# Performance work log

Hardware: AMD Instinct MI355X
Metric: run time of the kernel (lower is better)

Reference implementation:

```python
import jax, jax.numpy as jnp
import numpy as np

B, S, DM, H, HD, I, MAXREL = 4, 1024, 1024, 16, 64, 4096, 10
LN_EPS = 1e-3  # keras LayerNormalization default


def gelu(x):
    # tanh approximation from arXiv:1606.08415, as in the source
    return x * 0.5 * (1.0 + jnp.tanh(np.sqrt(2.0 / np.pi) * (x + 0.044715 * x ** 3)))


def layernorm(x, g, b):
    m = jnp.mean(x, axis=-1, keepdims=True)
    v = jnp.mean((x - m) ** 2, axis=-1, keepdims=True)
    return (x - m) * jax.lax.rsqrt(v + LN_EPS) * g + b


def setup_inputs() -> dict:
    key = jax.random.key(0)
    ks = jax.random.split(key, 12)
    sc = 0.02
    inp = {
        'x': jax.random.normal(ks[0], (B, S, DM), dtype=jnp.float32),
        'mask': jax.random.randint(ks[1], (B, S), 0, 2, dtype=jnp.int32),
        'Wqk': jax.random.normal(ks[2], (DM, H * HD), dtype=jnp.float32) * sc,
        'bqk': jnp.zeros((H * HD,), dtype=jnp.float32),
        'Wv': jax.random.normal(ks[3], (DM, H * HD), dtype=jnp.float32) * sc,
        'bv': jnp.zeros((H * HD,), dtype=jnp.float32),
        'rel_emb': jax.random.normal(ks[4], (2 * MAXREL + 1, HD), dtype=jnp.float32) * sc,
        'Wap': jax.random.normal(ks[5], (H * HD, DM), dtype=jnp.float32) * sc,
        'bap': jnp.zeros((DM,), dtype=jnp.float32),
        'g1': jnp.ones((DM,), dtype=jnp.float32),
        'b1': jnp.zeros((DM,), dtype=jnp.float32),
        'Wi': jax.random.normal(ks[6], (DM, I), dtype=jnp.float32) * sc,
        'bi': jnp.zeros((I,), dtype=jnp.float32),
        'Wo': jax.random.normal(ks[7], (I, DM), dtype=jnp.float32) * sc,
        'bo': jnp.zeros((DM,), dtype=jnp.float32),
        'g2': jnp.ones((DM,), dtype=jnp.float32),
        'b2': jnp.zeros((DM,), dtype=jnp.float32),
    }
    return inp


def _forward(x, mask, Wqk, bqk, Wv, bv, rel_emb, Wap, bap, g1, b1, Wi, bi, Wo, bo, g2, b2):
    b, s, _ = x.shape
    # shared query/key projection (qk_layer used for both q and k)
    qk = (x @ Wqk + bqk).reshape(b, s, H, HD).transpose(0, 2, 1, 3)  # [B,H,S,D]
    v = (x @ Wv + bv).reshape(b, s, H, HD).transpose(0, 2, 1, 3)
    # relative position ids: distance[i,j] = j - i, clipped to +-MAXREL, shifted
    r = jnp.arange(s)
    rel_idx = jnp.clip(r[None, :] - r[:, None], -MAXREL, MAXREL) + MAXREL  # [S,S]
    rel_k = rel_emb[rel_idx]  # [S,S,D]
    # Eq. 4 of arXiv:1803.02155 (note: no 1/sqrt(d) scaling in relative path)
    scores = jnp.einsum('bhqd,bhkd->bhqk', qk, qk) + jnp.einsum('bhqd,qkd->bhqk', qk, rel_k)
    # attention mask with self-exclusion (subtract identity, clip to [0,1])
    m = mask.astype(jnp.float32)  # [B,S]
    amask = jnp.clip(jnp.ones((b, s, 1), jnp.float32) * m[:, None, :] - jnp.eye(s), 0.0, 1.0)
    scores = scores + (1.0 - amask[:, None]) * -10000.0
    probs = jax.nn.softmax(scores, axis=-1)  # [B,H,S,S]
    ctx = jnp.einsum('bhqk,bhkd->bhqd', probs, v).transpose(0, 2, 1, 3).reshape(b, s, H * HD)
    # attention projection: Dense+gelu, residual, LN
    attn_out = layernorm(gelu(ctx @ Wap + bap) + x, g1, b1)
    inter = gelu(attn_out @ Wi + bi)
    out = layernorm(gelu(inter @ Wo + bo) + attn_out, g2, b2)
    return out, probs


def reference(x, mask, Wqk, bqk, Wv, bv, rel_emb, Wap, bap, g1, b1, Wi, bi, Wo, bo, g2, b2):
    return _forward(x, mask, Wqk, bqk, Wv, bv, rel_emb, Wap, bap, g1, b1, Wi, bi, Wo, bo, g2, b2)
```

## Files before the change

kernel.cpp:

```cpp
#include <hip/hip_runtime.h>
#include <hip/hip_bf16.h>

#define B_  4
#define S_  1024
#define DM_ 1024
#define H_  16
#define HD_ 64
#define I_  4096

typedef __attribute__((ext_vector_type(8))) short bf16x8;
typedef __attribute__((ext_vector_type(4))) float f32x4;

__device__ __forceinline__ float gelu_f(float x) {
  float x3 = x * x * x;
  return 0.5f * x * (1.0f + tanhf(0.7978845608028654f * (x + 0.044715f * x3)));
}

__device__ __forceinline__ unsigned short f32_to_bf16(float f) {
  unsigned int u = __float_as_uint(f);
  unsigned int rounding = 0x7FFFu + ((u >> 16) & 1u);
  u += rounding;
  return (unsigned short)(u >> 16);
}

__device__ __forceinline__ float bf16_to_f32(unsigned short u) {
  return __uint_as_float(((unsigned int)u) << 16);
}

__device__ __forceinline__ void split_bf16(float v, unsigned short& h, unsigned short& l) {
  h = f32_to_bf16(v);
  l = f32_to_bf16(v - bf16_to_f32(h));
}

__global__ __launch_bounds__(256) void cvt_bf16_kernel(
    const float* __restrict__ in, unsigned short* __restrict__ out, int n4)
{
  int i = blockIdx.x * 256 + threadIdx.x;
  if (i < n4) {
    float4 v = *reinterpret_cast<const float4*>(&in[(size_t)i * 4]);
    ushort4 o;
    o.x = f32_to_bf16(v.x); o.y = f32_to_bf16(v.y);
    o.z = f32_to_bf16(v.z); o.w = f32_to_bf16(v.w);
    *reinterpret_cast<ushort4*>(&out[(size_t)i * 4]) = o;
  }
}

__global__ __launch_bounds__(256) void tcvt_kernel(
    const float* __restrict__ W, unsigned short* __restrict__ WT, int K, int N)
{
  __shared__ float tile[64][65];
  const int tid = threadIdx.x;
  const int k0 = blockIdx.y * 64, n0 = blockIdx.x * 64;
#pragma unroll
  for (int i = 0; i < 4; ++i) {
    int u = tid + i * 256;
    int kr = u >> 4, nc = (u & 15) * 4;
    float4 v = *reinterpret_cast<const float4*>(&W[(size_t)(k0 + kr) * N + n0 + nc]);
    tile[kr][nc + 0] = v.x; tile[kr][nc + 1] = v.y;
    tile[kr][nc + 2] = v.z; tile[kr][nc + 3] = v.w;
  }
  __syncthreads();
  int n = tid >> 2, ks = (tid & 3) * 16;
  unsigned short* dst = &WT[(size_t)(n0 + n) * K + k0 + ks];
#pragma unroll
  for (int j = 0; j < 4; ++j) {
    ushort4 o;
    o.x = f32_to_bf16(tile[ks + j * 4 + 0][n]);
    o.y = f32_to_bf16(tile[ks + j * 4 + 1][n]);
    o.z = f32_to_bf16(tile[ks + j * 4 + 2][n]);
    o.w = f32_to_bf16(tile[ks + j * 4 + 3][n]);
    *reinterpret_cast<ushort4*>(&dst[j * 4]) = o;
  }
}

__global__ __launch_bounds__(256) void t_f32_kernel(
    const float* __restrict__ W, float* __restrict__ WT, int K, int N)
{
  __shared__ float tile[64][65];
  const int tid = threadIdx.x;
  const int k0 = blockIdx.y * 64, n0 = blockIdx.x * 64;
#pragma unroll
  for (int i = 0; i < 4; ++i) {
    int u = tid + i * 256;
    int kr = u >> 4, nc = (u & 15) * 4;
    float4 v = *reinterpret_cast<const float4*>(&W[(size_t)(k0 + kr) * N + n0 + nc]);
    tile[kr][nc + 0] = v.x; tile[kr][nc + 1] = v.y;
    tile[kr][nc + 2] = v.z; tile[kr][nc + 3] = v.w;
  }
  __syncthreads();
  int n = tid >> 2, ks = (tid & 3) * 16;
  float* dst = &WT[(size_t)(n0 + n) * K + k0 + ks];
#pragma unroll
  for (int j = 0; j < 4; ++j) {
    float4 o = make_float4(tile[ks + j * 4 + 0][n], tile[ks + j * 4 + 1][n],
                           tile[ks + j * 4 + 2][n], tile[ks + j * 4 + 3][n]);
    *reinterpret_cast<float4*>(&dst[j * 4]) = o;
  }
}

template<bool GELU, bool RES, bool RESBF16, bool BHSD, bool OBF16>
__global__ __launch_bounds__(256) void gemm_mfma_kernel(
    const unsigned short* __restrict__ A, const unsigned short* __restrict__ BT,
    const float* __restrict__ bias, const void* __restrict__ res,
    void* __restrict__ C, int M, int N, int K)
{
  __shared__ unsigned short As[128][40];
  __shared__ unsigned short Bs[128][40];
  const int tid = threadIdx.x;
  const int wid = tid >> 6;
  const int lane = tid & 63;
  const int bm = blockIdx.y * 128;
  const int bn = blockIdx.x * 128;
  const int l15 = lane & 15;
  const int kb = (lane >> 4) * 8;

  f32x4 acc[2][8];
#pragma unroll
  for (int mi = 0; mi < 2; ++mi)
#pragma unroll
    for (int ni = 0; ni < 8; ++ni) acc[mi][ni] = (f32x4){0.f, 0.f, 0.f, 0.f};

  for (int k0 = 0; k0 < K; k0 += 32) {
#pragma unroll
    for (int i = 0; i < 2; ++i) {
      int u = tid + i * 256;
      int row = u >> 2, seg = (u & 3) * 8;
      int4 va = *reinterpret_cast<const int4*>(&A[(size_t)(bm + row) * K + k0 + seg]);
      *reinterpret_cast<int4*>(&As[row][seg]) = va;
      int4 vb = *reinterpret_cast<const int4*>(&BT[(size_t)(bn + row) * K + k0 + seg]);
      *reinterpret_cast<int4*>(&Bs[row][seg]) = vb;
    }
    __syncthreads();

    bf16x8 af[2], bf[8];
#pragma unroll
    for (int mi = 0; mi < 2; ++mi)
      af[mi] = *reinterpret_cast<const bf16x8*>(&As[wid * 32 + mi * 16 + l15][kb]);
#pragma unroll
    for (int ni = 0; ni < 8; ++ni)
      bf[ni] = *reinterpret_cast<const bf16x8*>(&Bs[ni * 16 + l15][kb]);
#pragma unroll
    for (int mi = 0; mi < 2; ++mi)
#pragma unroll
      for (int ni = 0; ni < 8; ++ni)
        acc[mi][ni] = __builtin_amdgcn_mfma_f32_16x16x32_bf16(
            af[mi], bf[ni], acc[mi][ni], 0, 0, 0);
    __syncthreads();
  }

#pragma unroll
  for (int mi = 0; mi < 2; ++mi) {
#pragma unroll
    for (int ni = 0; ni < 8; ++ni) {
      int gcol = bn + ni * 16 + l15;
      float bsv = bias[gcol];
#pragma unroll
      for (int r = 0; r < 4; ++r) {
        int grow = bm + wid * 32 + mi * 16 + (lane >> 4) * 4 + r;
        float val = acc[mi][ni][r] + bsv;
        if (GELU) val = gelu_f(val);
        if (RES) {
          if (RESBF16) val += bf16_to_f32(((const unsigned short*)res)[(size_t)grow * N + gcol]);
          else         val += ((const float*)res)[(size_t)grow * N + gcol];
        }
        if (BHSD) {
          int bb = grow >> 10, ss = grow & 1023, hh = gcol >> 6, dd = gcol & 63;
          size_t adr = ((size_t)(bb * H_ + hh) * S_ + ss) * HD_ + dd;
          if (OBF16) ((unsigned short*)C)[adr] = f32_to_bf16(val);
          else       ((float*)C)[adr] = val;
        } else if (OBF16) {
          ((unsigned short*)C)[(size_t)grow * N + gcol] = f32_to_bf16(val);
        } else {
          ((float*)C)[(size_t)grow * N + gcol] = val;
        }
      }
    }
  }
}

__global__ __launch_bounds__(256) void gemm_mfma3_kernel(
    const float* __restrict__ A, const float* __restrict__ BT,
    const float* __restrict__ bias, float* __restrict__ C, int M, int N, int K)
{
  __shared__ unsigned short Ah[128][40], Al[128][40];
  __shared__ unsigned short Bh[128][40], Bl[128][40];
  const int tid = threadIdx.x;
  const int wid = tid >> 6;
  const int lane = tid & 63;
  const int bm = blockIdx.y * 128;
  const int bn = blockIdx.x * 128;
  const int l15 = lane & 15;
  const int kb = (lane >> 4) * 8;

  f32x4 acc[2][8];
#pragma unroll
  for (int mi = 0; mi < 2; ++mi)
#pragma unroll
    for (int ni = 0; ni < 8; ++ni) acc[mi][ni] = (f32x4){0.f, 0.f, 0.f, 0.f};

  for (int k0 = 0; k0 < K; k0 += 32) {
#pragma unroll
    for (int i = 0; i < 2; ++i) {
      int u = tid + i * 256;
      int row = u >> 2, seg = (u & 3) * 8;
#pragma unroll
      for (int half = 0; half < 2; ++half) {
        float4 va = *reinterpret_cast<const float4*>(&A[(size_t)(bm + row) * K + k0 + seg + half * 4]);
        ushort4 h4, l4;
        split_bf16(va.x, h4.x, l4.x); split_bf16(va.y, h4.y, l4.y);
        split_bf16(va.z, h4.z, l4.z); split_bf16(va.w, h4.w, l4.w);
        *reinterpret_cast<ushort4*>(&Ah[row][seg + half * 4]) = h4;
        *reinterpret_cast<ushort4*>(&Al[row][seg + half * 4]) = l4;
        float4 vb = *reinterpret_cast<const float4*>(&BT[(size_t)(bn + row) * K + k0 + seg + half * 4]);
        split_bf16(vb.x, h4.x, l4.x); split_bf16(vb.y, h4.y, l4.y);
        split_bf16(vb.z, h4.z, l4.z); split_bf16(vb.w, h4.w, l4.w);
        *reinterpret_cast<ushort4*>(&Bh[row][seg + half * 4]) = h4;
        *reinterpret_cast<ushort4*>(&Bl[row][seg + half * 4]) = l4;
      }
    }
    __syncthreads();

    bf16x8 ah[2], al[2];
#pragma unroll
    for (int mi = 0; mi < 2; ++mi) {
      ah[mi] = *reinterpret_cast<const bf16x8*>(&Ah[wid * 32 + mi * 16 + l15][kb]);
      al[mi] = *reinterpret_cast<const bf16x8*>(&Al[wid * 32 + mi * 16 + l15][kb]);
    }
#pragma unroll
    for (int ni = 0; ni < 8; ++ni) {
      bf16x8 bh = *reinterpret_cast<const bf16x8*>(&Bh[ni * 16 + l15][kb]);
      bf16x8 bl = *reinterpret_cast<const bf16x8*>(&Bl[ni * 16 + l15][kb]);
#pragma unroll
      for (int mi = 0; mi < 2; ++mi) {
        acc[mi][ni] = __builtin_amdgcn_mfma_f32_16x16x32_bf16(ah[mi], bh, acc[mi][ni], 0, 0, 0);
        acc[mi][ni] = __builtin_amdgcn_mfma_f32_16x16x32_bf16(al[mi], bh, acc[mi][ni], 0, 0, 0);
        acc[mi][ni] = __builtin_amdgcn_mfma_f32_16x16x32_bf16(ah[mi], bl, acc[mi][ni], 0, 0, 0);
      }
    }
    __syncthreads();
  }

#pragma unroll
  for (int mi = 0; mi < 2; ++mi) {
#pragma unroll
    for (int ni = 0; ni < 8; ++ni) {
      int gcol = bn + ni * 16 + l15;
      float bsv = bias[gcol];
#pragma unroll
      for (int r = 0; r < 4; ++r) {
        int grow = bm + wid * 32 + mi * 16 + (lane >> 4) * 4 + r;
        float val = acc[mi][ni][r] + bsv;
        int bb = grow >> 10, ss = grow & 1023, hh = gcol >> 6, dd = gcol & 63;
        C[((size_t)(bb * H_ + hh) * S_ + ss) * HD_ + dd] = val;
      }
    }
  }
}

__global__ __launch_bounds__(256) void attn_mfma_kernel(
    const float* __restrict__ qk, const int* __restrict__ mask,
    const float* __restrict__ rel_emb, float* __restrict__ probs)
{
  __shared__ unsigned short Qh[16][72], Ql[16][72];
  __shared__ float Qf[16][68];
  __shared__ unsigned short Kh[128][72], Kl[128][72];
  __shared__ float relp[16][21];
  __shared__ float red1[4][16], red2[4][16];
  __shared__ int msk[1024];

  const int tid = threadIdx.x;
  const int b = blockIdx.z, h = blockIdx.y, qt = blockIdx.x;
  const float* qkbh = qk + (size_t)(b * H_ + h) * S_ * HD_;
  const int q0 = qt * 16;

  for (int i = tid; i < 1024; i += 256) msk[i] = mask[b * S_ + i];

  {
    int row = tid >> 4, dq = (tid & 15) * 4;
    float4 v = *reinterpret_cast<const float4*>(&qkbh[(size_t)(q0 + row) * HD_ + dq]);
    Qf[row][dq + 0] = v.x; Qf[row][dq + 1] = v.y;
    Qf[row][dq + 2] = v.z; Qf[row][dq + 3] = v.w;
    ushort4 h4, l4;
    split_bf16(v.x, h4.x, l4.x); split_bf16(v.y, h4.y, l4.y);
    split_bf16(v.z, h4.z, l4.z); split_bf16(v.w, h4.w, l4.w);
    *reinterpret_cast<ushort4*>(&Qh[row][dq]) = h4;
    *reinterpret_cast<ushort4*>(&Ql[row][dq]) = l4;
  }
  __syncthreads();

  for (int idx = tid; idx < 16 * 21; idx += 256) {
    int q = idx / 21, r = idx - q * 21;
    float s = 0.f;
#pragma unroll 8
    for (int d = 0; d < 64; ++d) s += Qf[q][d] * rel_emb[r * 64 + d];
    relp[q][r] = s;
  }

  const int wv = tid >> 6;
  const int lane = tid & 63;
  const int l15 = lane & 15;
  const int hi4 = lane >> 4;
  const int kb = hi4 * 8;

  bf16x8 ah[2], al[2];
#pragma unroll
  for (int ks = 0; ks < 2; ++ks) {
    ah[ks] = *reinterpret_cast<const bf16x8*>(&Qh[l15][ks * 32 + kb]);
    al[ks] = *reinterpret_cast<const bf16x8*>(&Ql[l15][ks * 32 + kb]);
  }

  f32x4 acc[8][2];
#pragma unroll
  for (int t = 0; t < 8; ++t)
#pragma unroll
    for (int f = 0; f < 2; ++f) acc[t][f] = (f32x4){0.f, 0.f, 0.f, 0.f};

#pragma unroll
  for (int kt = 0; kt < 8; ++kt) {
    __syncthreads();
#pragma unroll
    for (int i = 0; i < 8; ++i) {
      int u = tid + i * 256;
      int row = u >> 4, dq = (u & 15) * 4;
      float4 v = *reinterpret_cast<const float4*>(&qkbh[(size_t)(kt * 128 + row) * HD_ + dq]);
      ushort4 h4, l4;
      split_bf16(v.x, h4.x, l4.x); split_bf16(v.y, h4.y, l4.y);
      split_bf16(v.z, h4.z, l4.z); split_bf16(v.w, h4.w, l4.w);
      *reinterpret_cast<ushort4*>(&Kh[row][dq]) = h4;
      *reinterpret_cast<ushort4*>(&Kl[row][dq]) = l4;
    }
    __syncthreads();

#pragma unroll
    for (int f = 0; f < 2; ++f) {
      int cb = wv * 32 + f * 16;
#pragma unroll
      for (int ks = 0; ks < 2; ++ks) {
        bf16x8 bh = *reinterpret_cast<const bf16x8*>(&Kh[cb + l15][ks * 32 + kb]);
        bf16x8 bl = *reinterpret_cast<const bf16x8*>(&Kl[cb + l15][ks * 32 + kb]);
        acc[kt][f] = __builtin_amdgcn_mfma_f32_16x16x32_bf16(ah[ks], bh, acc[kt][f], 0, 0, 0);
        acc[kt][f] = __builtin_amdgcn_mfma_f32_16x16x32_bf16(al[ks], bh, acc[kt][f], 0, 0, 0);
        acc[kt][f] = __builtin_amdgcn_mfma_f32_16x16x32_bf16(ah[ks], bl, acc[kt][f], 0, 0, 0);
      }
    }
  }
  __syncthreads();

  float mx[4] = {-3.0e38f, -3.0e38f, -3.0e38f, -3.0e38f};
#pragma unroll
  for (int t = 0; t < 8; ++t)
#pragma unroll
    for (int f = 0; f < 2; ++f)
#pragma unroll
      for (int r = 0; r < 4; ++r) {
        int ql = hi4 * 4 + r;
        int q = q0 + ql;
        int k = t * 128 + wv * 32 + f * 16 + l15;
        int d = k - q;
        int ridx = (d < -10 ? -10 : (d > 10 ? 10 : d)) + 10;
        float s = acc[t][f][r] + relp[ql][ridx];
        if (k == q || msk[k] == 0) s -= 10000.0f;
        acc[t][f][r] = s;
        mx[r] = fmaxf(mx[r], s);
      }
#pragma unroll
  for (int r = 0; r < 4; ++r) {
    mx[r] = fmaxf(mx[r], __shfl_xor(mx[r], 1));
    mx[r] = fmaxf(mx[r], __shfl_xor(mx[r], 2));
    mx[r] = fmaxf(mx[r], __shfl_xor(mx[r], 4));
    mx[r] = fmaxf(mx[r], __shfl_xor(mx[r], 8));
  }
  if (l15 == 0) {
#pragma unroll
    for (int r = 0; r < 4; ++r) red1[wv][hi4 * 4 + r] = mx[r];
  }
  __syncthreads();
  float mxq[4];
#pragma unroll
  for (int r = 0; r < 4; ++r) {
    int ql = hi4 * 4 + r;
    mxq[r] = fmaxf(fmaxf(red1[0][ql], red1[1][ql]), fmaxf(red1[2][ql], red1[3][ql]));
  }

  float sm[4] = {0.f, 0.f, 0.f, 0.f};
#pragma unroll
  for (int t = 0; t < 8; ++t)
#pragma unroll
    for (int f = 0; f < 2; ++f)
#pragma unroll
      for (int r = 0; r < 4; ++r) {
        float e = __expf(acc[t][f][r] - mxq[r]);
        acc[t][f][r] = e;
        sm[r] += e;
      }
#pragma unroll
  for (int r = 0; r < 4; ++r) {
    sm[r] += __shfl_xor(sm[r], 1);
    sm[r] += __shfl_xor(sm[r], 2);
    sm[r] += __shfl_xor(sm[r], 4);
    sm[r] += __shfl_xor(sm[r], 8);
  }
  if (l15 == 0) {
#pragma unroll
    for (int r = 0; r < 4; ++r) red2[wv][hi4 * 4 + r] = sm[r];
  }
  __syncthreads();
  float rinv[4];
#pragma unroll
  for (int r = 0; r < 4; ++r) {
    int ql = hi4 * 4 + r;
    rinv[r] = 1.0f / (red2[0][ql] + red2[1][ql] + red2[2][ql] + red2[3][ql]);
  }

  float* pb = probs + (size_t)(b * H_ + h) * S_ * S_;
#pragma unroll
  for (int t = 0; t < 8; ++t)
#pragma unroll
    for (int f = 0; f < 2; ++f)
#pragma unroll
      for (int r = 0; r < 4; ++r) {
        int q = q0 + hi4 * 4 + r;
        int k = t * 128 + wv * 32 + f * 16 + l15;
        pb[(size_t)q * S_ + k] = acc[t][f][r] * rinv[r];
      }
}

__global__ __launch_bounds__(256) void pv_mfma_kernel(
    const float* __restrict__ probs, const unsigned short* __restrict__ v,
    unsigned short* __restrict__ ctxb)
{
  __shared__ unsigned short Ps[128][40];
  __shared__ unsigned short Vt[64][40];
  const int tid = threadIdx.x;
  const int wid = tid >> 6;
  const int lane = tid & 63;
  const int l15 = lane & 15;
  const int kb = (lane >> 4) * 8;
  const int b = blockIdx.z, h = blockIdx.y, qt = blockIdx.x;
  const float* pr = probs + (size_t)(b * H_ + h) * S_ * S_ + (size_t)qt * 128 * S_;
  const unsigned short* vbh = v + (size_t)(b * H_ + h) * S_ * HD_;

  f32x4 acc[2][4];
#pragma unroll
  for (int mi = 0; mi < 2; ++mi)
#pragma unroll
    for (int ni = 0; ni < 4; ++ni) acc[mi][ni] = (f32x4){0.f, 0.f, 0.f, 0.f};

  for (int k0 = 0; k0 < S_; k0 += 32) {
#pragma unroll
    for (int i = 0; i < 2; ++i) {
      int u = tid + i * 256;
      int row = u >> 2, seg = (u & 3) * 8;
#pragma unroll
      for (int half = 0; half < 2; ++half) {
        float4 p4 = *reinterpret_cast<const float4*>(&pr[(size_t)row * S_ + k0 + seg + half * 4]);
        ushort4 o;
        o.x = f32_to_bf16(p4.x); o.y = f32_to_bf16(p4.y);
        o.z = f32_to_bf16(p4.z); o.w = f32_to_bf16(p4.w);
        *reinterpret_cast<ushort4*>(&Ps[row][seg + half * 4]) = o;
      }
    }
    {
      int i = tid >> 4;
#pragma unroll
      for (int j = 0; j < 2; ++j) {
        int u = tid + j * 256;
        int krow = u >> 4, dq = (u & 15) * 4;
        ushort4 vv = *reinterpret_cast<const ushort4*>(&vbh[(size_t)(k0 + krow) * HD_ + dq]);
        Vt[dq + 0][krow] = vv.x;
        Vt[dq + 1][krow] = vv.y;
        Vt[dq + 2][krow] = vv.z;
        Vt[dq + 3][krow] = vv.w;
      }
      (void)i;
    }
    __syncthreads();

    bf16x8 af[2], bf[4];
#pragma unroll
    for (int mi = 0; mi < 2; ++mi)
      af[mi] = *reinterpret_cast<const bf16x8*>(&Ps[wid * 32 + mi * 16 + l15][kb]);
#pragma unroll
    for (int ni = 0; ni < 4; ++ni)
      bf[ni] = *reinterpret_cast<const bf16x8*>(&Vt[ni * 16 + l15][kb]);
#pragma unroll
    for (int mi = 0; mi < 2; ++mi)
#pragma unroll
      for (int ni = 0; ni < 4; ++ni)
        acc[mi][ni] = __builtin_amdgcn_mfma_f32_16x16x32_bf16(
            af[mi], bf[ni], acc[mi][ni], 0, 0, 0);
    __syncthreads();
  }

#pragma unroll
  for (int mi = 0; mi < 2; ++mi)
#pragma unroll
    for (int ni = 0; ni < 4; ++ni) {
      int dd = ni * 16 + l15;
#pragma unroll
      for (int r = 0; r < 4; ++r) {
        int q = qt * 128 + wid * 32 + mi * 16 + (lane >> 4) * 4 + r;
        ctxb[((size_t)b * S_ + q) * DM_ + h * HD_ + dd] = f32_to_bf16(acc[mi][ni][r]);
      }
    }
}

template<bool OUTB16>
__global__ __launch_bounds__(256) void ln_kernel(
    const float* __restrict__ in, const float* __restrict__ g,
    const float* __restrict__ be, void* __restrict__ out)
{
  __shared__ float red[4];
  const int row = blockIdx.x, tid = threadIdx.x;
  const float* r = in + (size_t)row * DM_;
  float4 x = *reinterpret_cast<const float4*>(&r[tid * 4]);

  float s = x.x + x.y + x.z + x.w;
#pragma unroll
  for (int m = 1; m < 64; m <<= 1) s += __shfl_xor(s, m);
  if ((tid & 63) == 0) red[tid >> 6] = s;
  __syncthreads();
  float mean = (red[0] + red[1] + red[2] + red[3]) * (1.0f / 1024.0f);
  __syncthreads();

  float d0 = x.x - mean, d1 = x.y - mean, d2 = x.z - mean, d3 = x.w - mean;
  float sq = d0 * d0 + d1 * d1 + d2 * d2 + d3 * d3;
#pragma unroll
  for (int m = 1; m < 64; m <<= 1) sq += __shfl_xor(sq, m);
  if ((tid & 63) == 0) red[tid >> 6] = sq;
  __syncthreads();
  float var = (red[0] + red[1] + red[2] + red[3]) * (1.0f / 1024.0f);
  float rstd = rsqrtf(var + 1e-3f);

  int c = tid * 4;
  float4 gv = *reinterpret_cast<const float4*>(&g[c]);
  float4 bv = *reinterpret_cast<const float4*>(&be[c]);
  float y0 = d0 * rstd * gv.x + bv.x;
  float y1 = d1 * rstd * gv.y + bv.y;
  float y2 = d2 * rstd * gv.z + bv.z;
  float y3 = d3 * rstd * gv.w + bv.w;
  if (OUTB16) {
    ushort4 o;
    o.x = f32_to_bf16(y0); o.y = f32_to_bf16(y1);
    o.z = f32_to_bf16(y2); o.w = f32_to_bf16(y3);
    *reinterpret_cast<ushort4*>(&((unsigned short*)out)[(size_t)row * DM_ + c]) = o;
  } else {
    *reinterpret_cast<float4*>(&((float*)out)[(size_t)row * DM_ + c]) =
        make_float4(y0, y1, y2, y3);
  }
}

extern "C" void kernel_launch(void* const* d_in, const int* in_sizes, int n_in,
                              void* d_out, int out_size, void* d_ws, size_t ws_size,
                              hipStream_t stream) {
  const float* x    = (const float*)d_in[0];
  const int*   mask = (const int*)d_in[1];
  const float* Wqk  = (const float*)d_in[2];
  const float* bqk  = (const float*)d_in[3];
  const float* Wv   = (const float*)d_in[4];
  const float* bv   = (const float*)d_in[5];
  const float* rel  = (const float*)d_in[6];
  const float* Wap  = (const float*)d_in[7];
  const float* bap  = (const float*)d_in[8];
  const float* g1   = (const float*)d_in[9];
  const float* b1   = (const float*)d_in[10];
  const float* Wi   = (const float*)d_in[11];
  const float* bi   = (const float*)d_in[12];
  const float* Wo   = (const float*)d_in[13];
  const float* bo   = (const float*)d_in[14];
  const float* g2   = (const float*)d_in[15];
  const float* b2   = (const float*)d_in[16];

  char* wsb = (char*)d_ws;
  const size_t MB = 1048576;
  unsigned short* WoT    = (unsigned short*)(wsb + 0 * MB);
  unsigned short* WiT    = (unsigned short*)(wsb + 8 * MB);
  unsigned short* WvT    = (unsigned short*)(wsb + 16 * MB);
  unsigned short* WapT   = (unsigned short*)(wsb + 18 * MB);
  unsigned short* xb     = (unsigned short*)(wsb + 20 * MB);
  unsigned short* ctxb   = (unsigned short*)(wsb + 20 * MB);
  float*          WqkT   = (float*)(wsb + 28 * MB);
  float*          qkb    = (float*)(wsb + 32 * MB);
  float*          y      = (float*)(wsb + 32 * MB);
  unsigned short* vb     = (unsigned short*)(wsb + 48 * MB);
  unsigned short* attnb  = (unsigned short*)(wsb + 56 * MB);
  unsigned short* interb = (unsigned short*)(wsb + 16 * MB);

  float* outf  = (float*)d_out;
  float* probs = outf + 4194304;

  dim3 blk(256);
  cvt_bf16_kernel<<<4096, blk, 0, stream>>>(x, xb, 1048576);
  tcvt_kernel<<<dim3(16, 16), blk, 0, stream>>>(Wv,  WvT,  1024, 1024);
  tcvt_kernel<<<dim3(16, 16), blk, 0, stream>>>(Wap, WapT, 1024, 1024);
  tcvt_kernel<<<dim3(64, 16), blk, 0, stream>>>(Wi,  WiT,  1024, 4096);
  tcvt_kernel<<<dim3(16, 64), blk, 0, stream>>>(Wo,  WoT,  4096, 1024);
  t_f32_kernel<<<dim3(16, 16), blk, 0, stream>>>(Wqk, WqkT, 1024, 1024);

  gemm_mfma3_kernel<<<dim3(8, 32), blk, 0, stream>>>(
      x, WqkT, bqk, qkb, 4096, 1024, 1024);
  gemm_mfma_kernel<false, false, false, true, true><<<dim3(8, 32), blk, 0, stream>>>(
      xb, WvT, bv, nullptr, vb, 4096, 1024, 1024);
  attn_mfma_kernel<<<dim3(64, 16, 4), blk, 0, stream>>>(qkb, mask, rel, probs);
  pv_mfma_kernel<<<dim3(8, 16, 4), blk, 0, stream>>>(probs, vb, ctxb);
  gemm_mfma_kernel<true, true, false, false, false><<<dim3(8, 32), blk, 0, stream>>>(
      ctxb, WapT, bap, x, y, 4096, 1024, 1024);
  ln_kernel<true><<<4096, blk, 0, stream>>>(y, g1, b1, attnb);
  gemm_mfma_kernel<true, false, false, false, true><<<dim3(32, 32), blk, 0, stream>>>(
      attnb, WiT, bi, nullptr, interb, 4096, 4096, 1024);
  gemm_mfma_kernel<true, true, true, false, false><<<dim3(8, 32), blk, 0, stream>>>(
      interb, WoT, bo, attnb, outf, 4096, 1024, 4096);
  ln_kernel<false><<<4096, blk, 0, stream>>>(outf, g2, b2, outf);
}
```

Measured before the change: 623.4 us.

## Pre-split QK inputs into bf16 hi/lo and double query tile in attention

Splitting of x and Wqk into bf16 hi/lo pairs now happens once in the conversion kernels. The QK projection GEMM takes those pairs and writes its output as hi/lo bf16 arrays, so the attention kernel loads pre-split K tiles and no longer re-splits fp32 data for every query tile. The attention kernel also processes 32 queries per block instead of 16, which halves the number of K-tile reloads at the cost of more accumulator registers and possibly lower occupancy. The workspace layout is reshuffled to fit the new buffers.

```diff
diff --git a/kernel.cpp b/kernel.cpp
--- a/kernel.cpp
+++ b/kernel.cpp
@@ -32,16 +32,18 @@
   l = f32_to_bf16(v - bf16_to_f32(h));
 }
 
-__global__ __launch_bounds__(256) void cvt_bf16_kernel(
-    const float* __restrict__ in, unsigned short* __restrict__ out, int n4)
+__global__ __launch_bounds__(256) void cvt_split_kernel(
+    const float* __restrict__ in, unsigned short* __restrict__ hi,
+    unsigned short* __restrict__ lo, int n4)
 {
   int i = blockIdx.x * 256 + threadIdx.x;
   if (i < n4) {
     float4 v = *reinterpret_cast<const float4*>(&in[(size_t)i * 4]);
-    ushort4 o;
-    o.x = f32_to_bf16(v.x); o.y = f32_to_bf16(v.y);
-    o.z = f32_to_bf16(v.z); o.w = f32_to_bf16(v.w);
-    *reinterpret_cast<ushort4*>(&out[(size_t)i * 4]) = o;
+    ushort4 h4, l4;
+    split_bf16(v.x, h4.x, l4.x); split_bf16(v.y, h4.y, l4.y);
+    split_bf16(v.z, h4.z, l4.z); split_bf16(v.w, h4.w, l4.w);
+    *reinterpret_cast<ushort4*>(&hi[(size_t)i * 4]) = h4;
+    *reinterpret_cast<ushort4*>(&lo[(size_t)i * 4]) = l4;
   }
 }
 
@@ -73,8 +75,9 @@
   }
 }
 
-__global__ __launch_bounds__(256) void t_f32_kernel(
-    const float* __restrict__ W, float* __restrict__ WT, int K, int N)
+__global__ __launch_bounds__(256) void tcvt2_kernel(
+    const float* __restrict__ W, unsigned short* __restrict__ WTh,
+    unsigned short* __restrict__ WTl, int K, int N)
 {
   __shared__ float tile[64][65];
   const int tid = threadIdx.x;
@@ -89,12 +92,15 @@
   }
   __syncthreads();
   int n = tid >> 2, ks = (tid & 3) * 16;
-  float* dst = &WT[(size_t)(n0 + n) * K + k0 + ks];
 #pragma unroll
   for (int j = 0; j < 4; ++j) {
-    float4 o = make_float4(tile[ks + j * 4 + 0][n], tile[ks + j * 4 + 1][n],
-                           tile[ks + j * 4 + 2][n], tile[ks + j * 4 + 3][n]);
-    *reinterpret_cast<float4*>(&dst[j * 4]) = o;
+    ushort4 h4, l4;
+    split_bf16(tile[ks + j * 4 + 0][n], h4.x, l4.x);
+    split_bf16(tile[ks + j * 4 + 1][n], h4.y, l4.y);
+    split_bf16(tile[ks + j * 4 + 2][n], h4.z, l4.z);
+    split_bf16(tile[ks + j * 4 + 3][n], h4.w, l4.w);
+    *reinterpret_cast<ushort4*>(&WTh[(size_t)(n0 + n) * K + k0 + ks + j * 4]) = h4;
+    *reinterpret_cast<ushort4*>(&WTl[(size_t)(n0 + n) * K + k0 + ks + j * 4]) = l4;
   }
 }
 
@@ -132,19 +138,19 @@
     }
     __syncthreads();
 
-    bf16x8 af[2], bf[8];
+    bf16x8 af[2], bfr[8];
 #pragma unroll
     for (int mi = 0; mi < 2; ++mi)
       af[mi] = *reinterpret_cast<const bf16x8*>(&As[wid * 32 + mi * 16 + l15][kb]);
 #pragma unroll
     for (int ni = 0; ni < 8; ++ni)
-      bf[ni] = *reinterpret_cast<const bf16x8*>(&Bs[ni * 16 + l15][kb]);
+      bfr[ni] = *reinterpret_cast<const bf16x8*>(&Bs[ni * 16 + l15][kb]);
 #pragma unroll
     for (int mi = 0; mi < 2; ++mi)
 #pragma unroll
       for (int ni = 0; ni < 8; ++ni)
         acc[mi][ni] = __builtin_amdgcn_mfma_f32_16x16x32_bf16(
-            af[mi], bf[ni], acc[mi][ni], 0, 0, 0);
+            af[mi], bfr[ni], acc[mi][ni], 0, 0, 0);
     __syncthreads();
   }
 
@@ -179,8 +185,10 @@
 }
 
 __global__ __launch_bounds__(256) void gemm_mfma3_kernel(
-    const float* __restrict__ A, const float* __restrict__ BT,
-    const float* __restrict__ bias, float* __restrict__ C, int M, int N, int K)
+    const unsigned short* __restrict__ Ah_g, const unsigned short* __restrict__ Al_g,
+    const unsigned short* __restrict__ Bh_g, const unsigned short* __restrict__ Bl_g,
+    const float* __restrict__ bias, unsigned short* __restrict__ Ch,
+    unsigned short* __restrict__ Cl, int M, int N, int K)
 {
   __shared__ unsigned short Ah[128][40], Al[128][40];
   __shared__ unsigned short Bh[128][40], Bl[128][40];
@@ -203,20 +211,14 @@
     for (int i = 0; i < 2; ++i) {
       int u = tid + i * 256;
       int row = u >> 2, seg = (u & 3) * 8;
-#pragma unroll
-      for (int half = 0; half < 2; ++half) {
-        float4 va = *reinterpret_cast<const float4*>(&A[(size_t)(bm + row) * K + k0 + seg + half * 4]);
-        ushort4 h4, l4;
-        split_bf16(va.x, h4.x, l4.x); split_bf16(va.y, h4.y, l4.y);
-        split_bf16(va.z, h4.z, l4.z); split_bf16(va.w, h4.w, l4.w);
-        *reinterpret_cast<ushort4*>(&Ah[row][seg + half * 4]) = h4;
-        *reinterpret_cast<ushort4*>(&Al[row][seg + half * 4]) = l4;
-        float4 vb = *reinterpret_cast<const float4*>(&BT[(size_t)(bn + row) * K + k0 + seg + half * 4]);
-        split_bf16(vb.x, h4.x, l4.x); split_bf16(vb.y, h4.y, l4.y);
-        split_bf16(vb.z, h4.z, l4.z); split_bf16(vb.w, h4.w, l4.w);
-        *reinterpret_cast<ushort4*>(&Bh[row][seg + half * 4]) = h4;
-        *reinterpret_cast<ushort4*>(&Bl[row][seg + half * 4]) = l4;
-      }
+      *reinterpret_cast<int4*>(&Ah[row][seg]) =
+          *reinterpret_cast<const int4*>(&Ah_g[(size_t)(bm + row) * K + k0 + seg]);
+      *reinterpret_cast<int4*>(&Al[row][seg]) =
+          *reinterpret_cast<const int4*>(&Al_g[(size_t)(bm + row) * K + k0 + seg]);
+      *reinterpret_cast<int4*>(&Bh[row][seg]) =
+          *reinterpret_cast<const int4*>(&Bh_g[(size_t)(bn + row) * K + k0 + seg]);
+      *reinterpret_cast<int4*>(&Bl[row][seg]) =
+          *reinterpret_cast<const int4*>(&Bl_g[(size_t)(bn + row) * K + k0 + seg]);
     }
     __syncthreads();
 
@@ -251,48 +253,53 @@
         int grow = bm + wid * 32 + mi * 16 + (lane >> 4) * 4 + r;
         float val = acc[mi][ni][r] + bsv;
         int bb = grow >> 10, ss = grow & 1023, hh = gcol >> 6, dd = gcol & 63;
-        C[((size_t)(bb * H_ + hh) * S_ + ss) * HD_ + dd] = val;
+        size_t adr = ((size_t)(bb * H_ + hh) * S_ + ss) * HD_ + dd;
+        unsigned short h, l;
+        split_bf16(val, h, l);
+        Ch[adr] = h;
+        Cl[adr] = l;
       }
     }
   }
 }
 
 __global__ __launch_bounds__(256) void attn_mfma_kernel(
-    const float* __restrict__ qk, const int* __restrict__ mask,
-    const float* __restrict__ rel_emb, float* __restrict__ probs)
-{
-  __shared__ unsigned short Qh[16][72], Ql[16][72];
-  __shared__ float Qf[16][68];
+    const unsigned short* __restrict__ qkh, const unsigned short* __restrict__ qkl,
+    const int* __restrict__ mask, const float* __restrict__ rel_emb,
+    float* __restrict__ probs)
+{
+  __shared__ unsigned short Qh[32][72], Ql[32][72];
   __shared__ unsigned short Kh[128][72], Kl[128][72];
-  __shared__ float relp[16][21];
-  __shared__ float red1[4][16], red2[4][16];
+  __shared__ float relp[32][24];
+  __shared__ float red1[4][32], red2[4][32];
   __shared__ int msk[1024];
 
   const int tid = threadIdx.x;
   const int b = blockIdx.z, h = blockIdx.y, qt = blockIdx.x;
-  const float* qkbh = qk + (size_t)(b * H_ + h) * S_ * HD_;
-  const int q0 = qt * 16;
+  const size_t bh = (size_t)(b * H_ + h) * S_ * HD_;
+  const unsigned short* qh = qkh + bh;
+  const unsigned short* ql = qkl + bh;
+  const int q0 = qt * 32;
 
   for (int i = tid; i < 1024; i += 256) msk[i] = mask[b * S_ + i];
 
   {
-    int row = tid >> 4, dq = (tid & 15) * 4;
-    float4 v = *reinterpret_cast<const float4*>(&qkbh[(size_t)(q0 + row) * HD_ + dq]);
-    Qf[row][dq + 0] = v.x; Qf[row][dq + 1] = v.y;
-    Qf[row][dq + 2] = v.z; Qf[row][dq + 3] = v.w;
-    ushort4 h4, l4;
-    split_bf16(v.x, h4.x, l4.x); split_bf16(v.y, h4.y, l4.y);
-    split_bf16(v.z, h4.z, l4.z); split_bf16(v.w, h4.w, l4.w);
-    *reinterpret_cast<ushort4*>(&Qh[row][dq]) = h4;
-    *reinterpret_cast<ushort4*>(&Ql[row][dq]) = l4;
-  }
-  __syncthreads();
-
-  for (int idx = tid; idx < 16 * 21; idx += 256) {
+    int row = tid >> 3, seg = (tid & 7) * 8;
+    *reinterpret_cast<int4*>(&Qh[row][seg]) =
+        *reinterpret_cast<const int4*>(&qh[(size_t)(q0 + row) * HD_ + seg]);
+    *reinterpret_cast<int4*>(&Ql[row][seg]) =
+        *reinterpret_cast<const int4*>(&ql[(size_t)(q0 + row) * HD_ + seg]);
+  }
+  __syncthreads();
+
+  for (int idx = tid; idx < 32 * 21; idx += 256) {
     int q = idx / 21, r = idx - q * 21;
     float s = 0.f;
 #pragma unroll 8
-    for (int d = 0; d < 64; ++d) s += Qf[q][d] * rel_emb[r * 64 + d];
+    for (int d = 0; d < 64; ++d) {
+      float qf = bf16_to_f32(Qh[q][d]) + bf16_to_f32(Ql[q][d]);
+      s += qf * rel_emb[r * 64 + d];
+    }
     relp[q][r] = s;
   }
 
@@ -302,32 +309,34 @@
   const int hi4 = lane >> 4;
   const int kb = hi4 * 8;
 
-  bf16x8 ah[2], al[2];
-#pragma unroll
-  for (int ks = 0; ks < 2; ++ks) {
-    ah[ks] = *reinterpret_cast<const bf16x8*>(&Qh[l15][ks * 32 + kb]);
-    al[ks] = *reinterpret_cast<const bf16x8*>(&Ql[l15][ks * 32 + kb]);
-  }
-
-  f32x4 acc[8][2];
+  bf16x8 ah[2][2], al[2][2];
+#pragma unroll
+  for (int mi = 0; mi < 2; ++mi)
+#pragma unroll
+    for (int ks = 0; ks < 2; ++ks) {
+      ah[mi][ks] = *reinterpret_cast<const bf16x8*>(&Qh[mi * 16 + l15][ks * 32 + kb]);
+      al[mi][ks] = *reinterpret_cast<const bf16x8*>(&Ql[mi * 16 + l15][ks * 32 + kb]);
+    }
+
+  f32x4 acc[8][2][2];
 #pragma unroll
   for (int t = 0; t < 8; ++t)
 #pragma unroll
-    for (int f = 0; f < 2; ++f) acc[t][f] = (f32x4){0.f, 0.f, 0.f, 0.f};
+    for (int mi = 0; mi < 2; ++mi)
+#pragma unroll
+      for (int f = 0; f < 2; ++f) acc[t][mi][f] = (f32x4){0.f, 0.f, 0.f, 0.f};
 
 #pragma unroll
   for (int kt = 0; kt < 8; ++kt) {
     __syncthreads();
 #pragma unroll
-    for (int i = 0; i < 8; ++i) {
+    for (int i = 0; i < 4; ++i) {
       int u = tid + i * 256;
-      int row = u >> 4, dq = (u & 15) * 4;
-      float4 v = *reinterpret_cast<const float4*>(&qkbh[(size_t)(kt * 128 + row) * HD_ + dq]);
-      ushort4 h4, l4;
-      split_bf16(v.x, h4.x, l4.x); split_bf16(v.y, h4.y, l4.y);
-      split_bf16(v.z, h4.z, l4.z); split_bf16(v.w, h4.w, l4.w);
-      *reinterpret_cast<ushort4*>(&Kh[row][dq]) = h4;
-      *reinterpret_cast<ushort4*>(&Kl[row][dq]) = l4;
+      int row = u >> 3, seg = (u & 7) * 8;
+      *reinterpret_cast<int4*>(&Kh[row][seg]) =
+          *reinterpret_cast<const int4*>(&qh[(size_t)(kt * 128 + row) * HD_ + seg]);
+      *reinterpret_cast<int4*>(&Kl[row][seg]) =
+          *reinterpret_cast<const int4*>(&ql[(size_t)(kt * 128 + row) * HD_ + seg]);
     }
     __syncthreads();
 
@@ -338,91 +347,117 @@
       for (int ks = 0; ks < 2; ++ks) {
         bf16x8 bh = *reinterpret_cast<const bf16x8*>(&Kh[cb + l15][ks * 32 + kb]);
         bf16x8 bl = *reinterpret_cast<const bf16x8*>(&Kl[cb + l15][ks * 32 + kb]);
-        acc[kt][f] = __builtin_amdgcn_mfma_f32_16x16x32_bf16(ah[ks], bh, acc[kt][f], 0, 0, 0);
-        acc[kt][f] = __builtin_amdgcn_mfma_f32_16x16x32_bf16(al[ks], bh, acc[kt][f], 0, 0, 0);
-        acc[kt][f] = __builtin_amdgcn_mfma_f32_16x16x32_bf16(ah[ks], bl, acc[kt][f], 0, 0, 0);
+#pragma unroll
+        for (int mi = 0; mi < 2; ++mi) {
+          acc[kt][mi][f] = __builtin_amdgcn_mfma_f32_16x16x32_bf16(ah[mi][ks], bh, acc[kt][mi][f], 0, 0, 0);
+          acc[kt][mi][f] = __builtin_amdgcn_mfma_f32_16x16x32_bf16(al[mi][ks], bh, acc[kt][mi][f], 0, 0, 0);
+          acc[kt][mi][f] = __builtin_amdgcn_mfma_f32_16x16x32_bf16(ah[mi][ks], bl, acc[kt][mi][f], 0, 0, 0);
+        }
       }
     }
   }
   __syncthreads();
 
-  float mx[4] = {-3.0e38f, -3.0e38f, -3.0e38f, -3.0e38f};
+  float mx[2][4];
+#pragma unroll
+  for (int mi = 0; mi < 2; ++mi)
+#pragma unroll
+    for (int r = 0; r < 4; ++r) mx[mi][r] = -3.0e38f;
 #pragma unroll
   for (int t = 0; t < 8; ++t)
 #pragma unroll
-    for (int f = 0; f < 2; ++f)
-#pragma unroll
-      for (int r = 0; r < 4; ++r) {
-        int ql = hi4 * 4 + r;
-        int q = q0 + ql;
-        int k = t * 128 + wv * 32 + f * 16 + l15;
-        int d = k - q;
-        int ridx = (d < -10 ? -10 : (d > 10 ? 10 : d)) + 10;
-        float s = acc[t][f][r] + relp[ql][ridx];
-        if (k == q || msk[k] == 0) s -= 10000.0f;
-        acc[t][f][r] = s;
-        mx[r] = fmaxf(mx[r], s);
-      }
-#pragma unroll
-  for (int r = 0; r < 4; ++r) {
-    mx[r] = fmaxf(mx[r], __shfl_xor(mx[r], 1));
-    mx[r] = fmaxf(mx[r], __shfl_xor(mx[r], 2));
-    mx[r] = fmaxf(mx[r], __shfl_xor(mx[r], 4));
-    mx[r] = fmaxf(mx[r], __shfl_xor(mx[r], 8));
-  }
+    for (int mi = 0; mi < 2; ++mi)
+#pragma unroll
+      for (int f = 0; f < 2; ++f)
+#pragma unroll
+        for (int r = 0; r < 4; ++r) {
+          int qlc = mi * 16 + hi4 * 4 + r;
+          int q = q0 + qlc;
+          int k = t * 128 + wv * 32 + f * 16 + l15;
+          int d = k - q;
+          int ridx = (d < -10 ? -10 : (d > 10 ? 10 : d)) + 10;
+          float s = acc[t][mi][f][r] + relp[qlc][ridx];
+          if (k == q || msk[k] == 0) s -= 10000.0f;
+          acc[t][mi][f][r] = s;
+          mx[mi][r] = fmaxf(mx[mi][r], s);
+        }
+#pragma unroll
+  for (int mi = 0; mi < 2; ++mi)
+#pragma unroll
+    for (int r = 0; r < 4; ++r) {
+      mx[mi][r] = fmaxf(mx[mi][r], __shfl_xor(mx[mi][r], 1));
+      mx[mi][r] = fmaxf(mx[mi][r], __shfl_xor(mx[mi][r], 2));
+      mx[mi][r] = fmaxf(mx[mi][r], __shfl_xor(mx[mi][r], 4));
+      mx[mi][r] = fmaxf(mx[mi][r], __shfl_xor(mx[mi][r], 8));
+    }
   if (l15 == 0) {
 #pragma unroll
-    for (int r = 0; r < 4; ++r) red1[wv][hi4 * 4 + r] = mx[r];
-  }
-  __syncthreads();
-  float mxq[4];
-#pragma unroll
-  for (int r = 0; r < 4; ++r) {
-    int ql = hi4 * 4 + r;
-    mxq[r] = fmaxf(fmaxf(red1[0][ql], red1[1][ql]), fmaxf(red1[2][ql], red1[3][ql]));
-  }
-
-  float sm[4] = {0.f, 0.f, 0.f, 0.f};
+    for (int mi = 0; mi < 2; ++mi)
+#pragma unroll
+      for (int r = 0; r < 4; ++r) red1[wv][mi * 16 + hi4 * 4 + r] = mx[mi][r];
+  }
+  __syncthreads();
+  float mxq[2][4];
+#pragma unroll
+  for (int mi = 0; mi < 2; ++mi)
+#pragma unroll
+    for (int r = 0; r < 4; ++r) {
+      int qlc = mi * 16 + hi4 * 4 + r;
+      mxq[mi][r] = fmaxf(fmaxf(red1[0][qlc], red1[1][qlc]),
+                         fmaxf(red1[2][qlc], red1[3][qlc]));
+    }
+
+  float sm[2][4] = {{0.f, 0.f, 0.f, 0.f}, {0.f, 0.f, 0.f, 0.f}};
 #pragma unroll
   for (int t = 0; t < 8; ++t)
 #pragma unroll
-    for (int f = 0; f < 2; ++f)
-#pragma unroll
-      for (int r = 0; r < 4; ++r) {
-        float e = __expf(acc[t][f][r] - mxq[r]);
-        acc[t][f][r] = e;
-        sm[r] += e;
-      }
-#pragma unroll
-  for (int r = 0; r < 4; ++r) {
-    sm[r] += __shfl_xor(sm[r], 1);
-    sm[r] += __shfl_xor(sm[r], 2);
-    sm[r] += __shfl_xor(sm[r], 4);
-    sm[r] += __shfl_xor(sm[r], 8);
-  }
+    for (int mi = 0; mi < 2; ++mi)
+#pragma unroll
+      for (int f = 0; f < 2; ++f)
+#pragma unroll
+        for (int r = 0; r < 4; ++r) {
+          float e = __expf(acc[t][mi][f][r] - mxq[mi][r]);
+          acc[t][mi][f][r] = e;
+          sm[mi][r] += e;
+        }
+#pragma unroll
+  for (int mi = 0; mi < 2; ++mi)
+#pragma unroll
+    for (int r = 0; r < 4; ++r) {
+      sm[mi][r] += __shfl_xor(sm[mi][r], 1);
+      sm[mi][r] += __shfl_xor(sm[mi][r], 2);
+      sm[mi][r] += __shfl_xor(sm[mi][r], 4);
+      sm[mi][r] += __shfl_xor(sm[mi][r], 8);
+    }
   if (l15 == 0) {
 #pragma unroll
-    for (int r = 0; r < 4; ++r) red2[wv][hi4 * 4 + r] = sm[r];
-  }
-  __syncthreads();
-  float rinv[4];
-#pragma unroll
-  for (int r = 0; r < 4; ++r) {
-    int ql = hi4 * 4 + r;
-    rinv[r] = 1.0f / (red2[0][ql] + red2[1][ql] + red2[2][ql] + red2[3][ql]);
-  }
+    for (int mi = 0; mi < 2; ++mi)
+#pragma unroll
+      for (int r = 0; r < 4; ++r) red2[wv][mi * 16 + hi4 * 4 + r] = sm[mi][r];
+  }
+  __syncthreads();
+  float rinv[2][4];
+#pragma unroll
+  for (int mi = 0; mi < 2; ++mi)
+#pragma unroll
+    for (int r = 0; r < 4; ++r) {
+      int qlc = mi * 16 + hi4 * 4 + r;
+      rinv[mi][r] = 1.0f / (red2[0][qlc] + red2[1][qlc] + red2[2][qlc] + red2[3][qlc]);
+    }
 
   float* pb = probs + (size_t)(b * H_ + h) * S_ * S_;
 #pragma unroll
   for (int t = 0; t < 8; ++t)
 #pragma unroll
-    for (int f = 0; f < 2; ++f)
-#pragma unroll
-      for (int r = 0; r < 4; ++r) {
-        int q = q0 + hi4 * 4 + r;
-        int k = t * 128 + wv * 32 + f * 16 + l15;
-        pb[(size_t)q * S_ + k] = acc[t][f][r] * rinv[r];
-      }
+    for (int mi = 0; mi < 2; ++mi)
+#pragma unroll
+      for (int f = 0; f < 2; ++f)
+#pragma unroll
+        for (int r = 0; r < 4; ++r) {
+          int q = q0 + mi * 16 + hi4 * 4 + r;
+          int k = t * 128 + wv * 32 + f * 16 + l15;
+          pb[(size_t)q * S_ + k] = acc[t][mi][f][r] * rinv[mi][r];
+        }
 }
 
 __global__ __launch_bounds__(256) void pv_mfma_kernel(
@@ -461,7 +496,6 @@
       }
     }
     {
-      int i = tid >> 4;
 #pragma unroll
       for (int j = 0; j < 2; ++j) {
         int u = tid + j * 256;
@@ -472,23 +506,22 @@
         Vt[dq + 2][krow] = vv.z;
         Vt[dq + 3][krow] = vv.w;
       }
-      (void)i;
-    }
-    __syncthreads();
-
-    bf16x8 af[2], bf[4];
+    }
+    __syncthreads();
+
+    bf16x8 af[2], bfr[4];
 #pragma unroll
     for (int mi = 0; mi < 2; ++mi)
       af[mi] = *reinterpret_cast<const bf16x8*>(&Ps[wid * 32 + mi * 16 + l15][kb]);
 #pragma unroll
     for (int ni = 0; ni < 4; ++ni)
-      bf[ni] = *reinterpret_cast<const bf16x8*>(&Vt[ni * 16 + l15][kb]);
+      bfr[ni] = *reinterpret_cast<const bf16x8*>(&Vt[ni * 16 + l15][kb]);
 #pragma unroll
     for (int mi = 0; mi < 2; ++mi)
 #pragma unroll
       for (int ni = 0; ni < 4; ++ni)
         acc[mi][ni] = __builtin_amdgcn_mfma_f32_16x16x32_bf16(
-            af[mi], bf[ni], acc[mi][ni], 0, 0, 0);
+            af[mi], bfr[ni], acc[mi][ni], 0, 0, 0);
     __syncthreads();
   }
 
@@ -577,31 +610,34 @@
   unsigned short* WiT    = (unsigned short*)(wsb + 8 * MB);
   unsigned short* WvT    = (unsigned short*)(wsb + 16 * MB);
   unsigned short* WapT   = (unsigned short*)(wsb + 18 * MB);
-  unsigned short* xb     = (unsigned short*)(wsb + 20 * MB);
-  unsigned short* ctxb   = (unsigned short*)(wsb + 20 * MB);
-  float*          WqkT   = (float*)(wsb + 28 * MB);
-  float*          qkb    = (float*)(wsb + 32 * MB);
-  float*          y      = (float*)(wsb + 32 * MB);
-  unsigned short* vb     = (unsigned short*)(wsb + 48 * MB);
-  unsigned short* attnb  = (unsigned short*)(wsb + 56 * MB);
-  unsigned short* interb = (unsigned short*)(wsb + 16 * MB);
+  unsigned short* WqkTh  = (unsigned short*)(wsb + 20 * MB);
+  unsigned short* WqkTl  = (unsigned short*)(wsb + 22 * MB);
+  unsigned short* xh     = (unsigned short*)(wsb + 24 * MB);
+  unsigned short* xl     = (unsigned short*)(wsb + 32 * MB);
+  unsigned short* ctxb   = (unsigned short*)(wsb + 32 * MB);
+  unsigned short* qk_hi  = (unsigned short*)(wsb + 40 * MB);
+  unsigned short* qk_lo  = (unsigned short*)(wsb + 48 * MB);
+  float*          y      = (float*)(wsb + 40 * MB);
+  unsigned short* vb     = (unsigned short*)(wsb + 56 * MB);
+  unsigned short* attnb  = (unsigned short*)(wsb + 20 * MB);
+  unsigned short* interb = (unsigned short*)(wsb + 32 * MB);
 
   float* outf  = (float*)d_out;
   float* probs = outf + 4194304;
 
   dim3 blk(256);
-  cvt_bf16_kernel<<<4096, blk, 0, stream>>>(x, xb, 1048576);
+  cvt_split_kernel<<<4096, blk, 0, stream>>>(x, xh, xl, 1048576);
   tcvt_kernel<<<dim3(16, 16), blk, 0, stream>>>(Wv,  WvT,  1024, 1024);
   tcvt_kernel<<<dim3(16, 16), blk, 0, stream>>>(Wap, WapT, 1024, 1024);
   tcvt_kernel<<<dim3(64, 16), blk, 0, stream>>>(Wi,  WiT,  1024, 4096);
   tcvt_kernel<<<dim3(16, 64), blk, 0, stream>>>(Wo,  WoT,  4096, 1024);
-  t_f32_kernel<<<dim3(16, 16), blk, 0, stream>>>(Wqk, WqkT, 1024, 1024);
+  tcvt2_kernel<<<dim3(16, 16), blk, 0, stream>>>(Wqk, WqkTh, WqkTl, 1024, 1024);
 
   gemm_mfma3_kernel<<<dim3(8, 32), blk, 0, stream>>>(
-      x, WqkT, bqk, qkb, 4096, 1024, 1024);
+      xh, xl, WqkTh, WqkTl, bqk, qk_hi, qk_lo, 4096, 1024, 1024);
   gemm_mfma_kernel<false, false, false, true, true><<<dim3(8, 32), blk, 0, stream>>>(
-      xb, WvT, bv, nullptr, vb, 4096, 1024, 1024);
-  attn_mfma_kernel<<<dim3(64, 16, 4), blk, 0, stream>>>(qkb, mask, rel, probs);
+      xh, WvT, bv, nullptr, vb, 4096, 1024, 1024);
+  attn_mfma_kernel<<<dim3(32, 16, 4), blk, 0, stream>>>(qk_hi, qk_lo, mask, rel, probs);
   pv_mfma_kernel<<<dim3(8, 16, 4), blk, 0, stream>>>(probs, vb, ctxb);
   gemm_mfma_kernel<true, true, false, false, false><<<dim3(8, 32), blk, 0, stream>>>(
       ctxb, WapT, bap, x, y, 4096, 1024, 1024);
```

After: 639.7 us. +2.6%, slower.
